# Kernel tuning notes

Measured on AMD Instinct MI355X. Metric: run time of the kernel, lower is better.

Reference implementation:

```python
import jax, jax.numpy as jnp
import numpy as np


def setup_inputs() -> dict:
    key = jax.random.key(0)
    k1, k2 = jax.random.split(key)
    B, N, D = 8, 256, 128
    x = jax.random.normal(k1, (B, N, D), dtype=jnp.float32)
    # Dense edge layer: maps 2D -> D (concat of the two node embeddings).
    W = jax.random.normal(k2, (2 * D, D), dtype=jnp.float32) * (1.0 / np.sqrt(2 * D))
    b = jnp.zeros((D,), dtype=jnp.float32)
    return {"x": x, "W": W, "b": b}


def reference(x, W, b):
    # PairwiseEdgeEmbeddings: e[b,i,j] = concat(x[b,i], x[b,j])  -> (B,N,N,2D)
    # Edge layer: relu(e @ W + b)                                 -> (B,N,N,D)
    # Faithful but efficient: concat @ W == x_i @ W1 + x_j @ W2 with W=[W1;W2],
    # avoiding materializing the (B,N,N,2D) concat tensor.
    D = x.shape[-1]
    W1, W2 = W[:D], W[D:]
    a = jnp.einsum('bnd,df->bnf', x, W1)  # contribution of node i
    c = jnp.einsum('bnd,df->bnf', x, W2)  # contribution of node j
    edges = jax.nn.relu(a[:, :, None, :] + c[:, None, :, :] + b)  # (B,N,N,D)
    # Reduce layer: sum over j -> node embeddings (B,N,D)
    return edges.sum(axis=2)
```

## Files before the change

### kernel.cpp

```cpp
#include <hip/hip_runtime.h>

typedef float f32x4 __attribute__((ext_vector_type(4)));

#define B_ 8
#define N_ 256
#define D_ 128

__global__ __launch_bounds__(512) void sorted_relational_kernel(
    const float* __restrict__ x, const float* __restrict__ W,
    const float* __restrict__ bias, float* __restrict__ out) {

    __shared__ float Wc[256][4];
    __shared__ float CS[4][256];
    __shared__ float S0[4][257];
    __shared__ float S1[4][257];

    const int tid = threadIdx.x;
    const int bid = blockIdx.x;
    const int b   = bid & 7;
    const int f0  = (bid >> 3) * 4;

    if (tid < 256) {
        *reinterpret_cast<f32x4*>(&Wc[tid][0]) =
            *reinterpret_cast<const f32x4*>(W + (size_t)tid * D_ + f0);
    }
    __syncthreads();

    const int r    = tid & 255;
    const int half = tid >> 8;
    const float* __restrict__ xr = x + ((size_t)b * N_ + r) * D_;

    f32x4 acc = {0.f, 0.f, 0.f, 0.f};
    #pragma unroll 8
    for (int d4 = 0; d4 < 32; ++d4) {
        const f32x4 xv = *reinterpret_cast<const f32x4*>(xr + d4 * 4);
        const int wb = half * 128 + d4 * 4;
        const f32x4 w0 = *reinterpret_cast<const f32x4*>(&Wc[wb + 0][0]);
        const f32x4 w1 = *reinterpret_cast<const f32x4*>(&Wc[wb + 1][0]);
        const f32x4 w2 = *reinterpret_cast<const f32x4*>(&Wc[wb + 2][0]);
        const f32x4 w3 = *reinterpret_cast<const f32x4*>(&Wc[wb + 3][0]);
        acc += xv.x * w0 + xv.y * w1 + xv.z * w2 + xv.w * w3;
    }

    if (half) {
        CS[0][r] = acc[0]; CS[1][r] = acc[1];
        CS[2][r] = acc[2]; CS[3][r] = acc[3];
    } else {
        acc += *reinterpret_cast<const f32x4*>(bias + f0);
    }
    __syncthreads();

    {
        const int col = tid >> 7;
        const int m   = tid & 127;
        for (int k = 2; k <= 256; k <<= 1) {
            for (int j = k >> 1; j > 0; j >>= 1) {
                const int i = ((m & ~(j - 1)) << 1) | (m & (j - 1));
                const int p = i | j;
                const bool asc = (i & k) == 0;
                const float vi = CS[col][i];
                const float vp = CS[col][p];
                if ((vi > vp) == asc) {
                    CS[col][i] = vp;
                    CS[col][p] = vi;
                }
                __syncthreads();
            }
        }
    }

    {
        const int col = tid >> 7;
        const int m   = tid & 127;
        S0[col][m]       = CS[col][m];
        S0[col][m + 128] = CS[col][m + 128];
        if (m == 0) { S0[col][256] = 0.f; S1[col][256] = 0.f; }
        __syncthreads();

        float (*src)[257] = S0;
        float (*dst)[257] = S1;
        for (int d = 1; d <= 128; d <<= 1) {
            const int i0 = m, i1 = m + 128;
            const float v0 = src[col][i0] + (i0 + d < 256 ? src[col][i0 + d] : 0.f);
            const float v1 = src[col][i1] + (i1 + d < 256 ? src[col][i1 + d] : 0.f);
            dst[col][i0] = v0;
            dst[col][i1] = v1;
            __syncthreads();
            float (*t)[257] = src; src = dst; dst = t;
        }
    }

    if (half == 0) {
        float res[4];
        #pragma unroll
        for (int c = 0; c < 4; ++c) {
            const float a  = acc[c];
            const float na = -a;
            int lo = 0, hi = 256;
            #pragma unroll
            for (int it = 0; it < 8; ++it) {
                const int mid = (lo + hi) >> 1;
                if (CS[c][mid] > na) hi = mid; else lo = mid + 1;
            }
            const float K = (float)(256 - lo);
            const float S = S0[c][lo];
            res[c] = a * K + S;
        }
        f32x4 o = {res[0], res[1], res[2], res[3]};
        *reinterpret_cast<f32x4*>(out + ((size_t)b * N_ + r) * D_ + f0) = o;
    }
}

extern "C" void kernel_launch(void* const* d_in, const int* in_sizes, int n_in,
                              void* d_out, int out_size, void* d_ws, size_t ws_size,
                              hipStream_t stream) {
    const float* x    = (const float*)d_in[0];
    const float* W    = (const float*)d_in[1];
    const float* bias = (const float*)d_in[2];
    float* out = (float*)d_out;

    sorted_relational_kernel<<<B_ * (D_ / 4), 512, 0, stream>>>(x, W, bias, out);
}
```

Measured before the change: 19.70 us.

## Replace sort, prefix-sum and binary search with direct brute-force ReLU sum over j

The bitonic sort of the c column, the suffix-sum scan and the per-row binary search are replaced by a direct O(N^2) loop. Each thread computes relu(a_i + c_j) over half of the j values using vector max, and the two halves are combined through shared memory. This drops dozens of __syncthreads barriers and divergent compare-swap steps in exchange for about 128 vec4 add/max operations per thread, reading broadcast LDS values.

```diff
diff --git a/kernel.cpp b/kernel.cpp
--- a/kernel.cpp
+++ b/kernel.cpp
@@ -6,14 +6,14 @@
 #define N_ 256
 #define D_ 128
 
-__global__ __launch_bounds__(512) void sorted_relational_kernel(
+__global__ __launch_bounds__(512) void onepass_relational_kernel(
     const float* __restrict__ x, const float* __restrict__ W,
     const float* __restrict__ bias, float* __restrict__ out) {
 
-    __shared__ float Wc[256][4];
-    __shared__ float CS[4][256];
-    __shared__ float S0[4][257];
-    __shared__ float S1[4][257];
+    __shared__ f32x4 Wc[256];
+    __shared__ f32x4 AS[256];
+    __shared__ f32x4 CS[256];
+    __shared__ f32x4 PR[256];
 
     const int tid = threadIdx.x;
     const int bid = blockIdx.x;
@@ -21,93 +21,44 @@
     const int f0  = (bid >> 3) * 4;
 
     if (tid < 256) {
-        *reinterpret_cast<f32x4*>(&Wc[tid][0]) =
-            *reinterpret_cast<const f32x4*>(W + (size_t)tid * D_ + f0);
+        Wc[tid] = *reinterpret_cast<const f32x4*>(W + (size_t)tid * D_ + f0);
     }
     __syncthreads();
 
     const int r    = tid & 255;
     const int half = tid >> 8;
     const float* __restrict__ xr = x + ((size_t)b * N_ + r) * D_;
+    const f32x4* __restrict__ Wh = &Wc[half * 128];
 
     f32x4 acc = {0.f, 0.f, 0.f, 0.f};
     #pragma unroll 8
     for (int d4 = 0; d4 < 32; ++d4) {
         const f32x4 xv = *reinterpret_cast<const f32x4*>(xr + d4 * 4);
-        const int wb = half * 128 + d4 * 4;
-        const f32x4 w0 = *reinterpret_cast<const f32x4*>(&Wc[wb + 0][0]);
-        const f32x4 w1 = *reinterpret_cast<const f32x4*>(&Wc[wb + 1][0]);
-        const f32x4 w2 = *reinterpret_cast<const f32x4*>(&Wc[wb + 2][0]);
-        const f32x4 w3 = *reinterpret_cast<const f32x4*>(&Wc[wb + 3][0]);
-        acc += xv.x * w0 + xv.y * w1 + xv.z * w2 + xv.w * w3;
+        acc += xv[0] * Wh[d4 * 4 + 0] + xv[1] * Wh[d4 * 4 + 1] +
+               xv[2] * Wh[d4 * 4 + 2] + xv[3] * Wh[d4 * 4 + 3];
     }
 
     if (half) {
-        CS[0][r] = acc[0]; CS[1][r] = acc[1];
-        CS[2][r] = acc[2]; CS[3][r] = acc[3];
+        CS[r] = acc;
     } else {
-        acc += *reinterpret_cast<const f32x4*>(bias + f0);
+        AS[r] = acc + *reinterpret_cast<const f32x4*>(bias + f0);
     }
     __syncthreads();
 
-    {
-        const int col = tid >> 7;
-        const int m   = tid & 127;
-        for (int k = 2; k <= 256; k <<= 1) {
-            for (int j = k >> 1; j > 0; j >>= 1) {
-                const int i = ((m & ~(j - 1)) << 1) | (m & (j - 1));
-                const int p = i | j;
-                const bool asc = (i & k) == 0;
-                const float vi = CS[col][i];
-                const float vp = CS[col][p];
-                if ((vi > vp) == asc) {
-                    CS[col][i] = vp;
-                    CS[col][p] = vi;
-                }
-                __syncthreads();
-            }
-        }
+    const f32x4 zero = {0.f, 0.f, 0.f, 0.f};
+    const f32x4 av = AS[r];
+    const f32x4* __restrict__ Cj = &CS[half * 128];
+    f32x4 s = zero;
+    #pragma unroll 8
+    for (int j = 0; j < 128; ++j) {
+        s += __builtin_elementwise_max(av + Cj[j], zero);
     }
 
-    {
-        const int col = tid >> 7;
-        const int m   = tid & 127;
-        S0[col][m]       = CS[col][m];
-        S0[col][m + 128] = CS[col][m + 128];
-        if (m == 0) { S0[col][256] = 0.f; S1[col][256] = 0.f; }
-        __syncthreads();
-
-        float (*src)[257] = S0;
-        float (*dst)[257] = S1;
-        for (int d = 1; d <= 128; d <<= 1) {
-            const int i0 = m, i1 = m + 128;
-            const float v0 = src[col][i0] + (i0 + d < 256 ? src[col][i0 + d] : 0.f);
-            const float v1 = src[col][i1] + (i1 + d < 256 ? src[col][i1 + d] : 0.f);
-            dst[col][i0] = v0;
-            dst[col][i1] = v1;
-            __syncthreads();
-            float (*t)[257] = src; src = dst; dst = t;
-        }
-    }
-
-    if (half == 0) {
-        float res[4];
-        #pragma unroll
-        for (int c = 0; c < 4; ++c) {
-            const float a  = acc[c];
-            const float na = -a;
-            int lo = 0, hi = 256;
-            #pragma unroll
-            for (int it = 0; it < 8; ++it) {
-                const int mid = (lo + hi) >> 1;
-                if (CS[c][mid] > na) hi = mid; else lo = mid + 1;
-            }
-            const float K = (float)(256 - lo);
-            const float S = S0[c][lo];
-            res[c] = a * K + S;
-        }
-        f32x4 o = {res[0], res[1], res[2], res[3]};
-        *reinterpret_cast<f32x4*>(out + ((size_t)b * N_ + r) * D_ + f0) = o;
+    if (half) PR[r] = s;
+    __syncthreads();
+    if (!half) {
+        s += PR[r];
+        *reinterpret_cast<f32x4*>(out + ((size_t)b * N_ + r) * D_ + f0) = s;
     }
 }
 
@@ -119,5 +70,5 @@
     const float* bias = (const float*)d_in[2];
     float* out = (float*)d_out;
 
-    sorted_relational_kernel<<<B_ * (D_ / 4), 512, 0, stream>>>(x, W, bias, out);
+    onepass_relational_kernel<<<B_ * (D_ / 4), 512, 0, stream>>>(x, W, bias, out);
 }
```

New measurement: 19.27 us (median of 2 runs). 2.2% less time.
